# Kernel optimization log

Hardware: AMD Instinct MI355X
Metric: run time of the kernel (lower is better)

Reference implementation:

```python
import jax, jax.numpy as jnp
import numpy as np

EMBED_DIM = 1024
N_HEADS = 16


def setup_inputs() -> dict:
    key = jax.random.key(0)
    k1, k2, k3 = jax.random.split(key, 3)
    B, T, C = 4, 2048, EMBED_DIM
    x0 = jax.random.normal(k1, (B, T, C), dtype=jnp.float32)
    # Linear weights stored as (in, out) so y = x @ W, matching torch Linear math.
    w_attn = jax.random.normal(k2, (C, 3 * C), dtype=jnp.float32) * (1.0 / np.sqrt(C))
    w_proj = jax.random.normal(k3, (C, C), dtype=jnp.float32) * (1.0 / np.sqrt(C))
    return {"x0": x0, "w_attn": w_attn, "w_proj": w_proj}


def reference(x0, w_attn, w_proj):
    B, T, C = x0.shape
    H = N_HEADS
    D = C // H  # head dim
    qkv = x0 @ w_attn                      # [B, T, 3C]
    q, k, v = jnp.split(qkv, 3, axis=-1)
    # [B, T, C] -> [B, H, T, D]
    q = q.reshape(B, T, H, D).transpose(0, 2, 1, 3)
    k = k.reshape(B, T, H, D).transpose(0, 2, 1, 3)
    v = v.reshape(B, T, H, D).transpose(0, 2, 1, 3)
    scale = 1.0 / np.sqrt(D)
    attn = jnp.einsum('bhqd,bhkd->bhqk', q, k) * scale  # [B, H, T, T]
    causal = jnp.tril(jnp.ones((T, T), dtype=bool))
    attn = jnp.where(causal[None, None, :, :], attn, -jnp.inf)
    attn = jax.nn.softmax(attn, axis=-1)
    y = jnp.einsum('bhqk,bhkd->bhqd', attn, v)           # [B, H, T, D]
    y = y.transpose(0, 2, 1, 3).reshape(B, T, C)
    return y @ w_proj
```

## Files before the change

### kernel.cpp

```cpp
#include <hip/hip_runtime.h>

#define TSEQ 2048
#define NB 4
#define NH 16
#define HD 64
#define CEMB 1024
#define MROWS (NB*TSEQ)

typedef _Float16 half8 __attribute__((ext_vector_type(8)));
typedef _Float16 half4_t __attribute__((ext_vector_type(4)));
typedef float floatx4 __attribute__((ext_vector_type(4)));

__device__ __forceinline__ floatx4 mfma16x32(half8 a, half8 b, floatx4 c) {
    return __builtin_amdgcn_mfma_f32_16x16x32_f16(a, b, c, 0, 0, 0);
}

__device__ __forceinline__ void async16(const _Float16* g, _Float16* l) {
    __builtin_amdgcn_global_load_lds((const __attribute__((address_space(1))) void*)g,
                                     (__attribute__((address_space(3))) void*)l, 16, 0, 0);
}

__global__ __launch_bounds__(256) void cvt_fp32_fp16(const float* __restrict__ in,
                                                     _Float16* __restrict__ out) {
    size_t i = ((size_t)blockIdx.x * 256 + threadIdx.x) * 8;
    float4 a = *(const float4*)(in + i);
    float4 b = *(const float4*)(in + i + 4);
    half8 h;
    h[0] = (_Float16)a.x; h[1] = (_Float16)a.y; h[2] = (_Float16)a.z; h[3] = (_Float16)a.w;
    h[4] = (_Float16)b.x; h[5] = (_Float16)b.y; h[6] = (_Float16)b.z; h[7] = (_Float16)b.w;
    *(half8*)(out + i) = h;
}

__global__ __launch_bounds__(256) void transpose_cvt(const float* __restrict__ in,
                                                     _Float16* __restrict__ out,
                                                     int R, int Ccols) {
    __shared__ float tile[32][33];
    int bx = blockIdx.x;
    int by = blockIdx.y;
    int tx = threadIdx.x, ty = threadIdx.y;
    int x = bx * 32 + tx;
#pragma unroll
    for (int i = 0; i < 32; i += 8) {
        int y = by * 32 + ty + i;
        tile[ty + i][tx] = in[(size_t)y * Ccols + x];
    }
    __syncthreads();
#pragma unroll
    for (int i = 0; i < 32; i += 8) {
        int oc = bx * 32 + ty + i;
        int orow = by * 32 + tx;
        out[(size_t)oc * R + orow] = (_Float16)tile[tx][ty + i];
    }
}

template<int MODE, int BM>
__global__ __launch_bounds__(BM * 2, 4) void gemm_nt(const _Float16* __restrict__ A,
                                                     const _Float16* __restrict__ Bt,
                                                     float* __restrict__ Cf,
                                                     _Float16* __restrict__ Ch,
                                                     _Float16* __restrict__ VTh,
                                                     int N, int K) {
    __shared__ __align__(16) _Float16 As[2][BM * 32];
    __shared__ __align__(16) _Float16 Bs[2][4096];

    const int tid = threadIdx.x;
    const int wv = tid >> 6, lane = tid & 63;
    const int wm = (BM == 256) ? (wv & 3) : (wv >> 1);
    const int wn = (BM == 256) ? (wv >> 2) : (wv & 1);
    const int l16 = lane & 15, lq = lane >> 4;

    const int pid = blockIdx.x + gridDim.x * blockIdx.y;
    const int nn = gridDim.y;
    const int pig = 8 * nn;
    const int gid = pid / pig;
    const int rem = pid - gid * pig;
    const int bm = gid * 8 + (rem & 7);
    const int bn = rem >> 3;

    const int srow = lane >> 2;
    const int scol = ((lane & 3) ^ ((lane >> 3) & 3)) * 8;
    const _Float16* Abase = A + (size_t)(bm * BM) * K;
    const _Float16* Bbase = Bt + (size_t)(bn * 128) * K;

    const floatx4 zero = {0.f, 0.f, 0.f, 0.f};
    floatx4 acc[4][4];
#pragma unroll
    for (int i = 0; i < 4; i++)
#pragma unroll
        for (int j = 0; j < 4; j++) acc[i][j] = zero;

    auto stage = [&](int bf, int k0) {
#pragma unroll
        for (int cc = 0; cc < 2; cc++) {
            const int c = wv * 2 + cc;
            const size_t gofs = (size_t)(c * 16 + srow) * K + k0 + scol;
            async16(Abase + gofs, &As[bf][c * 512]);
        }
        if (BM == 256) {
            const int c = wv;
            const size_t gofs = (size_t)(c * 16 + srow) * K + k0 + scol;
            async16(Bbase + gofs, &Bs[bf][c * 512]);
        } else {
#pragma unroll
            for (int cc = 0; cc < 2; cc++) {
                const int c = wv * 2 + cc;
                const size_t gofs = (size_t)(c * 16 + srow) * K + k0 + scol;
                async16(Bbase + gofs, &Bs[bf][c * 512]);
            }
        }
    };

    stage(0, 0);
    int buf = 0;
    const int sw = (lq ^ ((l16 >> 1) & 3)) * 8;
    for (int k0 = 0; k0 < K; k0 += 32) {
        __syncthreads();
        if (k0 + 32 < K) stage(buf ^ 1, k0 + 32);
        half8 af[4], bf[4];
#pragma unroll
        for (int i = 0; i < 4; i++) {
            af[i] = *(const half8*)&As[buf][(wm * 64 + i * 16 + l16) * 32 + sw];
            bf[i] = *(const half8*)&Bs[buf][(wn * 64 + i * 16 + l16) * 32 + sw];
        }
#pragma unroll
        for (int i = 0; i < 4; i++)
#pragma unroll
            for (int j = 0; j < 4; j++)
                acc[i][j] = mfma16x32(af[i], bf[j], acc[i][j]);
        buf ^= 1;
    }

    if (MODE == 1) {
#pragma unroll
        for (int i = 0; i < 4; i++) {
            int row = bm * BM + wm * 64 + i * 16 + lq * 4;
#pragma unroll
            for (int j = 0; j < 4; j++) {
                int col = bn * 128 + wn * 64 + j * 16 + l16;
#pragma unroll
                for (int r = 0; r < 4; r++)
                    Cf[(size_t)(row + r) * N + col] = acc[i][j][r];
            }
        }
    } else {
        const int which = bn >> 3;
        if (which < 2) {
#pragma unroll
            for (int j = 0; j < 4; j++) {
                int n = bn * 128 + wn * 64 + j * 16 + l16;
                int c = n & 1023, h = c >> 6, d = c & 63;
                _Float16* dst = Ch + (size_t)which * ((size_t)MROWS * CEMB)
                                   + (size_t)h * (TSEQ * HD) + d;
#pragma unroll
                for (int i = 0; i < 4; i++) {
                    int row = bm * BM + wm * 64 + i * 16 + lq * 4;
#pragma unroll
                    for (int r = 0; r < 4; r++) {
                        int m = row + r;
                        int b = m >> 11, t = m & 2047;
                        dst[(size_t)b * (NH * TSEQ * HD) + (size_t)t * HD] = (_Float16)acc[i][j][r];
                    }
                }
            }
        } else {
#pragma unroll
            for (int j = 0; j < 4; j++) {
                int n = bn * 128 + wn * 64 + j * 16 + l16;
                int c = n & 1023, h = c >> 6, d = c & 63;
#pragma unroll
                for (int i = 0; i < 4; i++) {
                    int m0 = bm * BM + wm * 64 + i * 16 + lq * 4;
                    int b = m0 >> 11, t = m0 & 2047;
                    half4_t pk;
#pragma unroll
                    for (int r = 0; r < 4; r++) pk[r] = (_Float16)acc[i][j][r];
                    *(half4_t*)&VTh[(((size_t)(b * NH + h)) * HD + d) * TSEQ + t] = pk;
                }
            }
        }
    }
}

__global__ __launch_bounds__(512, 4) void attn_fwd(const _Float16* __restrict__ Qg,
                                                   const _Float16* __restrict__ Kg,
                                                   const _Float16* __restrict__ VTg,
                                                   _Float16* __restrict__ Y) {
    __shared__ __align__(16) _Float16 Ks[2][4096];
    __shared__ __align__(16) _Float16 Vt[2][4096];

    const int tid = threadIdx.x;
    const int w = tid >> 6, lane = tid & 63;
    const int l16 = lane & 15, quad = lane >> 4;
    const int bh = blockIdx.y;
    const int x = blockIdx.x;
    const int b = bh >> 4, h = bh & 15;
    const int qt = (b < 2) ? x : (7 - x);

    const _Float16* Qb = Qg + (size_t)bh * TSEQ * HD;
    const _Float16* Kb = Kg + (size_t)bh * TSEQ * HD;
    const _Float16* Vb = VTg + (size_t)bh * HD * TSEQ;

    const _Float16 ksc = (_Float16)(0.125f * 1.44269504089f);
    const floatx4 zero = {0.f, 0.f, 0.f, 0.f};

    half8 qf[2][2];
#pragma unroll
    for (int g = 0; g < 2; g++) {
        const _Float16* qrow = Qb + (size_t)(qt * 256 + g * 128 + w * 16 + l16) * HD;
        qf[g][0] = *(const half8*)(qrow + quad * 8);
        qf[g][1] = *(const half8*)(qrow + 32 + quad * 8);
#pragma unroll
        for (int e = 0; e < 8; e++) { qf[g][0][e] *= ksc; qf[g][1][e] *= ksc; }
    }

    floatx4 o[2][4];
#pragma unroll
    for (int g = 0; g < 2; g++)
#pragma unroll
        for (int dt = 0; dt < 4; dt++) o[g][dt] = zero;
    float lsum[2] = {0.f, 0.f};

    const int srow8 = lane >> 3;
    const int scol8 = ((lane & 7) ^ (lane >> 3)) * 8;

    auto stage = [&](int bf, int kt2) {
        const int row = w * 8 + srow8;
        async16(Kb + (size_t)(kt2 * 64 + row) * HD + scol8, &Ks[bf][w * 512]);
        async16(Vb + (size_t)row * TSEQ + kt2 * 64 + scol8, &Vt[bf][w * 512]);
    };

    const int kmax = 4 * qt + 3;
    stage(0, 0);
    int buf = 0;
    for (int kt = 0; kt <= kmax; ++kt) {
        __syncthreads();
        if (kt < kmax) stage(buf ^ 1, kt + 1);

        half8 kf0[4], kf1[4];
#pragma unroll
        for (int nj = 0; nj < 4; nj++) {
            const int rb = (nj * 16 + l16) * 64;
            kf0[nj] = *(const half8*)&Ks[buf][rb + ((quad ^ (l16 & 7)) * 8)];
            kf1[nj] = *(const half8*)&Ks[buf][rb + (((quad ^ 4) ^ (l16 & 7)) * 8)];
        }

        const bool doA = (kt <= 4 * qt + 1);
        half8 pf[2][2];
#pragma unroll
        for (int g = 0; g < 2; g++) {
            if (g == 0 && !doA) continue;
            floatx4 st[4];
#pragma unroll
            for (int nj = 0; nj < 4; nj++) {
                floatx4 t = mfma16x32(kf0[nj], qf[g][0], zero);
                st[nj] = mfma16x32(kf1[nj], qf[g][1], t);
            }
            if (kt * 64 + 63 > qt * 256 + g * 128 + w * 16) {
                const int klim = qt * 256 + g * 128 + w * 16 + l16 - kt * 64;
#pragma unroll
                for (int nj = 0; nj < 4; nj++)
#pragma unroll
                    for (int r = 0; r < 4; r++) {
                        int key = nj * 16 + quad * 4 + r;
                        if (key > klim) st[nj][r] = -1e30f;
                    }
            }
#pragma unroll
            for (int nj = 0; nj < 4; nj++)
#pragma unroll
                for (int r = 0; r < 4; r++) {
                    float p = __builtin_amdgcn_exp2f(st[nj][r]);
                    lsum[g] += p;
                    pf[g][nj >> 1][(nj & 1) * 4 + r] = (_Float16)p;
                }
        }

#pragma unroll
        for (int u = 0; u < 2; u++) {
#pragma unroll
            for (int dt = 0; dt < 4; dt++) {
                const int rb = (dt * 16 + l16) * 64;
                const int g0 = u * 4 + (quad >> 1);
                const int sub = (quad & 1) * 4;
                half4_t lo = *(const half4_t*)&Vt[buf][rb + ((g0 ^ (l16 & 7)) * 8 + sub)];
                half4_t hi = *(const half4_t*)&Vt[buf][rb + (((g0 + 2) ^ (l16 & 7)) * 8 + sub)];
                half8 vf;
                vf[0] = lo[0]; vf[1] = lo[1]; vf[2] = lo[2]; vf[3] = lo[3];
                vf[4] = hi[0]; vf[5] = hi[1]; vf[6] = hi[2]; vf[7] = hi[3];
                if (doA) o[0][dt] = mfma16x32(pf[0][u], vf, o[0][dt]);
                o[1][dt] = mfma16x32(pf[1][u], vf, o[1][dt]);
            }
        }
        buf ^= 1;
    }

#pragma unroll
    for (int g = 0; g < 2; g++) {
        float lt = lsum[g];
        lt += __shfl_xor(lt, 16);
        lt += __shfl_xor(lt, 32);
        float linv[4];
#pragma unroll
        for (int r = 0; r < 4; r++) linv[r] = 1.0f / __shfl(lt, quad * 4 + r);
#pragma unroll
        for (int dt = 0; dt < 4; dt++)
#pragma unroll
            for (int r = 0; r < 4; r++) {
                int q = qt * 256 + g * 128 + w * 16 + quad * 4 + r;
                int d = dt * 16 + l16;
                Y[((size_t)(b * TSEQ + q)) * CEMB + h * HD + d] = (_Float16)(o[g][dt][r] * linv[r]);
            }
    }
}

extern "C" void kernel_launch(void* const* d_in, const int* in_sizes, int n_in,
                              void* d_out, int out_size, void* d_ws, size_t ws_size,
                              hipStream_t stream) {
    const float* x0     = (const float*)d_in[0];
    const float* w_attn = (const float*)d_in[1];
    const float* w_proj = (const float*)d_in[2];
    float* out = (float*)d_out;

    _Float16* xh  = (_Float16*)d_ws;
    _Float16* wqt = xh  + (size_t)MROWS * CEMB;
    _Float16* wpt = wqt + (size_t)3 * CEMB * CEMB;
    _Float16* qh  = wpt + (size_t)CEMB * CEMB;
    _Float16* kh  = qh  + (size_t)MROWS * CEMB;
    _Float16* vt  = kh  + (size_t)MROWS * CEMB;
    _Float16* yh  = vt  + (size_t)MROWS * CEMB;

    cvt_fp32_fp16<<<(MROWS * CEMB) / (256 * 8), 256, 0, stream>>>(x0, xh);
    transpose_cvt<<<dim3(3 * CEMB / 32, CEMB / 32), dim3(32, 8), 0, stream>>>(w_attn, wqt, CEMB, 3 * CEMB);
    transpose_cvt<<<dim3(CEMB / 32, CEMB / 32), dim3(32, 8), 0, stream>>>(w_proj, wpt, CEMB, CEMB);

    gemm_nt<0, 256><<<dim3(MROWS / 256, 3 * CEMB / 128), 512, 0, stream>>>(xh, wqt, nullptr, qh, vt, 3 * CEMB, CEMB);
    attn_fwd<<<dim3(TSEQ / 256, NB * NH), 512, 0, stream>>>(qh, kh, vt, yh);
    gemm_nt<1, 128><<<dim3(MROWS / 128, CEMB / 128), 256, 0, stream>>>(yh, wpt, out, nullptr, nullptr, CEMB, CEMB);
}
```

Measured before the change: 249.1 us.

## Widen attention key tiles to 128 and merge prep kernels into one launch

The attention kernel now stages 128 keys per iteration instead of 64, with a 16-way XOR swizzle for the V tile. This halves the number of loop iterations and barriers per query tile, at the cost of doubling LDS use (64KB per block) and possibly lowering occupancy. Separately, the fp32-to-fp16 conversion of x and the two weight transposes are fused into one launch to cut launch overhead.

New measurement: 258.8 us. 1.04x slower.

```diff
diff --git a/kernel.cpp b/kernel.cpp
--- a/kernel.cpp
+++ b/kernel.cpp
@@ -20,25 +20,39 @@
                                      (__attribute__((address_space(3))) void*)l, 16, 0, 0);
 }
 
-__global__ __launch_bounds__(256) void cvt_fp32_fp16(const float* __restrict__ in,
-                                                     _Float16* __restrict__ out) {
-    size_t i = ((size_t)blockIdx.x * 256 + threadIdx.x) * 8;
-    float4 a = *(const float4*)(in + i);
-    float4 b = *(const float4*)(in + i + 4);
-    half8 h;
-    h[0] = (_Float16)a.x; h[1] = (_Float16)a.y; h[2] = (_Float16)a.z; h[3] = (_Float16)a.w;
-    h[4] = (_Float16)b.x; h[5] = (_Float16)b.y; h[6] = (_Float16)b.z; h[7] = (_Float16)b.w;
-    *(half8*)(out + i) = h;
-}
-
-__global__ __launch_bounds__(256) void transpose_cvt(const float* __restrict__ in,
-                                                     _Float16* __restrict__ out,
-                                                     int R, int Ccols) {
+__global__ __launch_bounds__(256) void prep(const float* __restrict__ x0,
+                                            const float* __restrict__ w_attn,
+                                            const float* __restrict__ w_proj,
+                                            _Float16* __restrict__ xh,
+                                            _Float16* __restrict__ wqt,
+                                            _Float16* __restrict__ wpt) {
     __shared__ float tile[32][33];
-    int bx = blockIdx.x;
-    int by = blockIdx.y;
-    int tx = threadIdx.x, ty = threadIdx.y;
-    int x = bx * 32 + tx;
+    const int id = blockIdx.x;
+    const int tid = threadIdx.x;
+    if (id < 4096) {
+        size_t i = ((size_t)id * 256 + tid) * 8;
+        float4 a = *(const float4*)(x0 + i);
+        float4 b = *(const float4*)(x0 + i + 4);
+        half8 h;
+        h[0] = (_Float16)a.x; h[1] = (_Float16)a.y; h[2] = (_Float16)a.z; h[3] = (_Float16)a.w;
+        h[4] = (_Float16)b.x; h[5] = (_Float16)b.y; h[6] = (_Float16)b.z; h[7] = (_Float16)b.w;
+        *(half8*)(xh + i) = h;
+        return;
+    }
+    const float* in;
+    _Float16* out;
+    int bx, by, R, Ccols;
+    if (id < 4096 + 3072) {
+        int id2 = id - 4096;
+        bx = id2 % 96; by = id2 / 96; R = CEMB; Ccols = 3 * CEMB;
+        in = w_attn; out = wqt;
+    } else {
+        int id2 = id - 7168;
+        bx = id2 % 32; by = id2 / 32; R = CEMB; Ccols = CEMB;
+        in = w_proj; out = wpt;
+    }
+    const int tx = tid & 31, ty = tid >> 5;
+    const int x = bx * 32 + tx;
 #pragma unroll
     for (int i = 0; i < 32; i += 8) {
         int y = by * 32 + ty + i;
@@ -185,8 +199,8 @@
                                                    const _Float16* __restrict__ Kg,
                                                    const _Float16* __restrict__ VTg,
                                                    _Float16* __restrict__ Y) {
-    __shared__ __align__(16) _Float16 Ks[2][4096];
-    __shared__ __align__(16) _Float16 Vt[2][4096];
+    __shared__ __align__(16) _Float16 Ks[2][8192];
+    __shared__ __align__(16) _Float16 Vt[2][8192];
 
     const int tid = threadIdx.x;
     const int w = tid >> 6, lane = tid & 63;
@@ -220,70 +234,70 @@
         for (int dt = 0; dt < 4; dt++) o[g][dt] = zero;
     float lsum[2] = {0.f, 0.f};
 
-    const int srow8 = lane >> 3;
-    const int scol8 = ((lane & 7) ^ (lane >> 3)) * 8;
+    const int krow = lane >> 3;
+    const int kcol = ((lane & 7) ^ (lane >> 3)) * 8;
+    const int vrow = lane >> 4;
+    const int vunit = lane & 15;
 
     auto stage = [&](int bf, int kt2) {
-        const int row = w * 8 + srow8;
-        async16(Kb + (size_t)(kt2 * 64 + row) * HD + scol8, &Ks[bf][w * 512]);
-        async16(Vb + (size_t)row * TSEQ + kt2 * 64 + scol8, &Vt[bf][w * 512]);
+#pragma unroll
+        for (int cc = 0; cc < 2; cc++) {
+            const int c = w * 2 + cc;
+            const int row = c * 8 + krow;
+            async16(Kb + (size_t)(kt2 * 128 + row) * HD + kcol, &Ks[bf][c * 512]);
+            const int d = c * 4 + vrow;
+            const int su = (vunit ^ (d & 15)) * 8;
+            async16(Vb + (size_t)d * TSEQ + kt2 * 128 + su, &Vt[bf][c * 512]);
+        }
     };
 
-    const int kmax = 4 * qt + 3;
+    const int kmax = 2 * qt + 1;
     stage(0, 0);
     int buf = 0;
     for (int kt = 0; kt <= kmax; ++kt) {
         __syncthreads();
         if (kt < kmax) stage(buf ^ 1, kt + 1);
 
-        half8 kf0[4], kf1[4];
-#pragma unroll
-        for (int nj = 0; nj < 4; nj++) {
-            const int rb = (nj * 16 + l16) * 64;
-            kf0[nj] = *(const half8*)&Ks[buf][rb + ((quad ^ (l16 & 7)) * 8)];
-            kf1[nj] = *(const half8*)&Ks[buf][rb + (((quad ^ 4) ^ (l16 & 7)) * 8)];
-        }
-
-        const bool doA = (kt <= 4 * qt + 1);
-        half8 pf[2][2];
+        const bool doA = (kt <= 2 * qt);
+        half8 pf[2][4];
 #pragma unroll
         for (int g = 0; g < 2; g++) {
             if (g == 0 && !doA) continue;
-            floatx4 st[4];
-#pragma unroll
-            for (int nj = 0; nj < 4; nj++) {
-                floatx4 t = mfma16x32(kf0[nj], qf[g][0], zero);
-                st[nj] = mfma16x32(kf1[nj], qf[g][1], t);
-            }
-            if (kt * 64 + 63 > qt * 256 + g * 128 + w * 16) {
-                const int klim = qt * 256 + g * 128 + w * 16 + l16 - kt * 64;
-#pragma unroll
-                for (int nj = 0; nj < 4; nj++)
+            const int qbase = qt * 256 + g * 128 + w * 16;
+            const bool maskT = (kt * 128 + 127 > qbase);
+            const int klim = qbase + l16 - kt * 128;
+#pragma unroll
+            for (int nj = 0; nj < 8; nj++) {
+                const int rb = (nj * 16 + l16) * 64;
+                half8 kf0 = *(const half8*)&Ks[buf][rb + ((quad ^ (l16 & 7)) * 8)];
+                half8 kf1 = *(const half8*)&Ks[buf][rb + (((quad ^ 4) ^ (l16 & 7)) * 8)];
+                floatx4 st = mfma16x32(kf0, qf[g][0], zero);
+                st = mfma16x32(kf1, qf[g][1], st);
+                if (maskT) {
 #pragma unroll
                     for (int r = 0; r < 4; r++) {
                         int key = nj * 16 + quad * 4 + r;
-                        if (key > klim) st[nj][r] = -1e30f;
+                        if (key > klim) st[r] = -1e30f;
                     }
-            }
-#pragma unroll
-            for (int nj = 0; nj < 4; nj++)
+                }
 #pragma unroll
                 for (int r = 0; r < 4; r++) {
-                    float p = __builtin_amdgcn_exp2f(st[nj][r]);
+                    float p = __builtin_amdgcn_exp2f(st[r]);
                     lsum[g] += p;
                     pf[g][nj >> 1][(nj & 1) * 4 + r] = (_Float16)p;
                 }
-        }
-
-#pragma unroll
-        for (int u = 0; u < 2; u++) {
+            }
+        }
+
+#pragma unroll
+        for (int u = 0; u < 4; u++) {
 #pragma unroll
             for (int dt = 0; dt < 4; dt++) {
-                const int rb = (dt * 16 + l16) * 64;
-                const int g0 = u * 4 + (quad >> 1);
+                const int rb = (dt * 16 + l16) * 128;
+                const int G0 = u * 4 + (quad >> 1);
                 const int sub = (quad & 1) * 4;
-                half4_t lo = *(const half4_t*)&Vt[buf][rb + ((g0 ^ (l16 & 7)) * 8 + sub)];
-                half4_t hi = *(const half4_t*)&Vt[buf][rb + (((g0 + 2) ^ (l16 & 7)) * 8 + sub)];
+                half4_t lo = *(const half4_t*)&Vt[buf][rb + (((G0) ^ (l16 & 15)) * 8 + sub)];
+                half4_t hi = *(const half4_t*)&Vt[buf][rb + (((G0 + 2) ^ (l16 & 15)) * 8 + sub)];
                 half8 vf;
                 vf[0] = lo[0]; vf[1] = lo[1]; vf[2] = lo[2]; vf[3] = lo[3];
                 vf[4] = hi[0]; vf[5] = hi[1]; vf[6] = hi[2]; vf[7] = hi[3];
@@ -329,10 +343,7 @@
     _Float16* vt  = kh  + (size_t)MROWS * CEMB;
     _Float16* yh  = vt  + (size_t)MROWS * CEMB;
 
-    cvt_fp32_fp16<<<(MROWS * CEMB) / (256 * 8), 256, 0, stream>>>(x0, xh);
-    transpose_cvt<<<dim3(3 * CEMB / 32, CEMB / 32), dim3(32, 8), 0, stream>>>(w_attn, wqt, CEMB, 3 * CEMB);
-    transpose_cvt<<<dim3(CEMB / 32, CEMB / 32), dim3(32, 8), 0, stream>>>(w_proj, wpt, CEMB, CEMB);
-
+    prep<<<4096 + 3072 + 1024, 256, 0, stream>>>(x0, w_attn, w_proj, xh, wqt, wpt);
     gemm_nt<0, 256><<<dim3(MROWS / 256, 3 * CEMB / 128), 512, 0, stream>>>(xh, wqt, nullptr, qh, vt, 3 * CEMB, CEMB);
     attn_fwd<<<dim3(TSEQ / 256, NB * NH), 512, 0, stream>>>(qh, kh, vt, yh);
     gemm_nt<1, 128><<<dim3(MROWS / 128, CEMB / 128), 256, 0, stream>>>(yh, wpt, out, nullptr, nullptr, CEMB, CEMB);
```
